# Performance work log

Measured on AMD Instinct MI355X. Metric: run time of the kernel, lower is better.

## Reference

```python
import jax, jax.numpy as jnp
import numpy as np

N_QUBITS = 16   # downsampled_size**2
N_KERNELS = 2
BSZ = 16        # hardcoded BATCH_SIZE in the repo
INV_SQRT2 = 0.70710678118654752


def ry_mat(theta):
    # RY(t) = [[cos(t/2), -sin(t/2)], [sin(t/2), cos(t/2)]]; theta: scalar or any batch shape
    c = jnp.cos(theta / 2)
    s = jnp.sin(theta / 2)
    m = jnp.stack([jnp.stack([c, -s], -1), jnp.stack([s, c], -1)], -2)
    return m.astype(jnp.complex64)


def rx_mat(theta):
    # RX(t) = [[cos(t/2), -i sin(t/2)], [-i sin(t/2), cos(t/2)]]
    c = jnp.cos(theta / 2).astype(jnp.complex64)
    s = jnp.sin(theta / 2).astype(jnp.complex64)
    return jnp.stack([jnp.stack([c, -1j * s], -1), jnp.stack([-1j * s, c], -1)], -2)


def apply_1q(state, U, w, n):
    # state: (b, 2**n) complex; U: (2,2) or (b,2,2); wire 0 = most significant bit
    b = state.shape[0]
    dl, dr = 1 << w, 1 << (n - 1 - w)
    s = state.reshape(b, dl, 2, dr)
    if U.ndim == 2:
        s = jnp.einsum('ab,xLbR->xLaR', U, s)
    else:
        s = jnp.einsum('xab,xLbR->xLaR', U, s)
    return s.reshape(b, -1)


def apply_cnot(state, c, t, n):
    # flip target axis where control bit == 1
    b = state.shape[0]
    st = state.reshape((b,) + (2,) * n)
    flipped = jnp.flip(st, axis=1 + t)
    mshape = [1] * (n + 1)
    mshape[1 + c] = 2
    ctrl = jnp.arange(2).reshape(mshape)
    st = jnp.where(ctrl == 1, flipped, st)
    return st.reshape(b, -1)


def quantum_model(xd, kernel_params):
    # xd: (b, 16) angles; kernel_params: (n_kernels, 5)
    b = xd.shape[0]
    n = N_QUBITS
    N = 1 << n
    bits = (jnp.arange(N)[:, None] >> jnp.arange(n - 1, -1, -1)[None, :]) & 1
    signs = (1 - 2 * bits).astype(jnp.float32)  # (N, n), PauliZ eigenvalues per wire
    enc = ry_mat(xd)  # (b, 16, 2, 2)
    outs = []
    for k in range(N_KERNELS):
        p = kernel_params[k]
        state = jnp.zeros((b, N), jnp.complex64).at[:, 0].set(1.0)
        # encoder: RY(x_i) on wire i
        for w in range(n):
            state = apply_1q(state, enc[:, w], w, n)
        # QuantumConvolution block (shared 5 trainable angles)
        ry0, ry1, ry2 = ry_mat(p[0]), ry_mat(p[1]), ry_mat(p[2])
        rx0, rx1 = rx_mat(p[3]), rx_mat(p[4])
        for i in range(n - 4):
            state = apply_1q(state, ry0, i, n)
            state = apply_cnot(state, i, i + 3, n)
            state = apply_1q(state, ry1, i + 3, n)
            state = apply_1q(state, ry2, i + 1, n)
            state = apply_cnot(state, i + 1, i + 4, n)
            state = apply_cnot(state, i + 3, i + 1, n)
            state = apply_1q(state, rx0, i + 4, n)
            state = apply_1q(state, rx1, i + 1, n)
        for i in range(n - 4):
            state = apply_cnot(state, i + 1, i, n)
            state = apply_cnot(state, i + 3, i, n)
            state = apply_cnot(state, i + 4, i, n)
        probs = state.real ** 2 + state.imag ** 2  # (b, N)
        expz = probs @ signs                        # (b, n)
        outs.append(expz[:, :-4])                   # drop last 4 wires
    return jnp.concatenate(outs, axis=1)            # (b, n_kernels*(n-4)) = (b, 24)


def setup_inputs() -> dict:
    key = jax.random.key(0)
    ks = jax.random.split(key, 8)
    return {
        'x': jax.random.normal(ks[0], (BSZ, 1, 28, 28), jnp.float32),
        'kernel_params': jax.random.uniform(ks[1], (N_KERNELS, 5), jnp.float32) * (2 * np.pi),
        'fc1_w': jax.random.normal(ks[2], (128, 24), jnp.float32) * 0.1,
        'fc1_b': jnp.zeros((128,), jnp.float32),
        'fc2_w': jax.random.normal(ks[3], (64, 128), jnp.float32) * 0.1,
        'fc2_b': jnp.zeros((64,), jnp.float32),
        'fc3_w': jax.random.normal(ks[4], (4, 64), jnp.float32) * 0.1,
        'fc3_b': jnp.zeros((4,), jnp.float32),
    }


def reference(x, kernel_params, fc1_w, fc1_b, fc2_w, fc2_b, fc3_w, fc3_b):
    b = x.shape[0]
    # AvgPool2d(kernel=7, stride=7): 28x28 -> 4x4, then flatten -> 16 features
    xd = x.reshape(b, 1, 4, 7, 4, 7).mean(axis=(3, 5)).reshape(b, 16)
    feats = quantum_model(xd, kernel_params)       # (b, 24)
    h = jax.nn.relu(feats @ fc1_w.T + fc1_b)
    h = jax.nn.relu(h @ fc2_w.T + fc2_b)
    return h @ fc3_w.T + fc3_b                      # (b, 4)
```

## Files before the change

kernel.cpp:

```cpp
#include <hip/hip_runtime.h>
#include <math.h>

typedef float2 cplx;
__device__ __forceinline__ cplx mk(float r, float i){ return make_float2(r, i); }

template<int B> struct LSH {
  static constexpr int v = (B==7)?0 : (B==8)?1 : (B==2)?2 : (B==1)?3 : (B==0)?4 : 5;
};

template<int PB>
__device__ __forceinline__ float lx(float v){
  if constexpr (PB == 7)
    return __int_as_float(__builtin_amdgcn_update_dpp(
        __float_as_int(v), __float_as_int(v), 0xB1, 0xF, 0xF, false));
  else if constexpr (PB == 8)
    return __int_as_float(__builtin_amdgcn_update_dpp(
        __float_as_int(v), __float_as_int(v), 0x4E, 0xF, 0xF, false));
  else if constexpr (PB == 2)
    return __int_as_float(__builtin_amdgcn_ds_swizzle(__float_as_int(v), 0x101F));
  else if constexpr (PB == 1)
    return __int_as_float(__builtin_amdgcn_ds_swizzle(__float_as_int(v), 0x201F));
  else if constexpr (PB == 0)
    return __int_as_float(__builtin_amdgcn_ds_swizzle(__float_as_int(v), 0x401F));
  else
    return __shfl_xor(v, 32, 64);
}

template<int PB, int CB, bool ISRX>
__device__ __forceinline__ void gate_pass(cplx* A, float c, float s, int lane)
{
  if constexpr (PB >= 3 && PB <= 6) {
    constexpr int RM = 1 << (PB - 3);
    bool cl = false;
    if constexpr (CB >= 0 && !(CB >= 3 && CB <= 6))
      cl = (lane >> LSH<CB>::v) & 1;
    #pragma unroll
    for (int r = 0; r < 16; ++r) {
      if (r & RM) continue;
      cplx a0 = A[r], a1 = A[r | RM];
      bool sw;
      if constexpr (CB < 0) sw = false;
      else if constexpr (CB >= 3 && CB <= 6) sw = (r >> (CB - 3)) & 1;
      else sw = cl;
      float i0x = sw ? a1.x : a0.x, i0y = sw ? a1.y : a0.y;
      float i1x = sw ? a0.x : a1.x, i1y = sw ? a0.y : a1.y;
      if constexpr (ISRX) {
        A[r]      = mk(fmaf(s, i1y, c*i0x), fmaf(-s, i1x, c*i0y));
        A[r | RM] = mk(fmaf(s, i0y, c*i1x), fmaf(-s, i0x, c*i1y));
      } else {
        A[r]      = mk(fmaf(-s, i1x, c*i0x), fmaf(-s, i1y, c*i0y));
        A[r | RM] = mk(fmaf( s, i0x, c*i1x), fmaf( s, i0y, c*i1y));
      }
    }
  } else {
    const int mybit = (lane >> LSH<PB>::v) & 1;
    const float ssy = mybit ? s : -s;
    #pragma unroll
    for (int r = 0; r < 16; ++r) {
      float px = lx<PB>(A[r].x);
      float py = lx<PB>(A[r].y);
      bool sw = false;
      if constexpr (CB >= 3 && CB <= 6) sw = (r >> (CB - 3)) & 1;
      float ox = A[r].x, oy = A[r].y;
      float ux = sw ? px : ox, uy = sw ? py : oy;
      float vx = sw ? ox : px, vy = sw ? oy : py;
      if constexpr (ISRX) A[r] = mk(fmaf(s, vy, c*ux), fmaf(-s, vx, c*uy));
      else                A[r] = mk(fmaf(ssy, vx, c*ux), fmaf(ssy, vy, c*uy));
    }
  }
}

template<int LO>
__device__ __forceinline__ void iter_reg(cplx* A, int lane,
    float c0,float s0,float c1,float s1,float c2,float s2,
    float cx,float sx,float c4,float s4)
{
  gate_pass<LO+4, -1,   false>(A, c0, s0, lane);
  gate_pass<LO+1, LO+4, false>(A, c1, s1, lane);
  gate_pass<LO+3, -1,   false>(A, c2, s2, lane);
  gate_pass<LO,   LO+3, true >(A, cx, sx, lane);
  gate_pass<LO+3, LO+1, true >(A, c4, s4, lane);
}

#define RUN6(A) \
  iter_reg<5>(A, lane, hc0,hs0,hc1,hs1,hc2,hs2,hcx,hsx,hc4,hs4); \
  iter_reg<4>(A, lane, hc0,hs0,hc1,hs1,hc2,hs2,hcx,hsx,hc4,hs4); \
  iter_reg<3>(A, lane, hc0,hs0,hc1,hs1,hc2,hs2,hcx,hsx,hc4,hs4); \
  iter_reg<2>(A, lane, hc0,hs0,hc1,hs1,hc2,hs2,hcx,hsx,hc4,hs4); \
  iter_reg<1>(A, lane, hc0,hs0,hc1,hs1,hc2,hs2,hcx,hsx,hc4,hs4); \
  iter_reg<0>(A, lane, hc0,hs0,hc1,hs1,hc2,hs2,hcx,hsx,hc4,hs4);

__device__ __forceinline__ float wave_sum(float v){
  v += lx<7>(v);
  v += lx<8>(v);
  v += lx<2>(v);
  v += lx<1>(v);
  v += lx<0>(v);
  v += __shfl_xor(v, 32, 64);
  return v;
}

__global__ __launch_bounds__(256) void sim_kernel(
    const float* __restrict__ x, const float* __restrict__ kp,
    float* __restrict__ pacc)
{
  __shared__ __align__(16) float lds[8320];

  const int tid = threadIdx.x, wv = tid >> 6, lane = tid & 63;
  const int gw = blockIdx.x * 4 + wv;
  const int pair = gw >> 6;
  const int chunk = gw & 63;
  const int b = pair & 15, k = pair >> 4;

  cplx*  P    = (cplx*)&lds[wv * 2048];
  float* angw = &lds[8192 + wv * 32];

  {
    int a = lane >> 2, q = lane & 3;
    int ii = a >> 2, jj = a & 3;
    const float* xb = x + b*784 + ii*7*28 + jj*7;
    float s = 0.f;
    for (int e = q; e < 49; e += 4) s += xb[(e/7)*28 + (e%7)];
    s += __shfl_xor(s, 1, 64);
    s += __shfl_xor(s, 2, 64);
    float ang = s * (1.0f/49.0f) * 0.5f;
    if (q == 0){ angw[a*2] = cosf(ang); angw[a*2+1] = sinf(ang); }
  }

  const float* p5 = kp + k*5;
  float hc0 = cosf(p5[0]*0.5f), hs0 = sinf(p5[0]*0.5f);
  float hc1 = cosf(p5[1]*0.5f), hs1 = sinf(p5[1]*0.5f);
  float hc2 = cosf(p5[2]*0.5f), hs2 = sinf(p5[2]*0.5f);
  float hcx = cosf(p5[3]*0.5f), hsx = sinf(p5[3]*0.5f);
  float hc4 = cosf(p5[4]*0.5f), hs4 = sinf(p5[4]*0.5f);

  __threadfence_block();

  cplx A[16];

  {
    float lp = 1.f;
    lp *= ((lane>>5)&1) ? angw[1]  : angw[0];
    lp *= ((lane>>1)&1) ? angw[3]  : angw[2];
    lp *= ( lane    &1) ? angw[5]  : angw[4];
    lp *= ((lane>>2)&1) ? angw[15] : angw[14];
    lp *= ((lane>>3)&1) ? angw[17] : angw[16];
    lp *= ((lane>>4)&1) ? angw[19] : angw[18];
    float c3 = angw[6],  s3 = angw[7];
    float c4w= angw[8],  s4w= angw[9];
    float c5 = angw[10], s5 = angw[11];
    float c6 = angw[12], s6 = angw[13];
    #pragma unroll
    for (int r = 0; r < 16; ++r){
      float rp = ((r&8)? s3:c3) * ((r&4)? s4w:c4w) * ((r&2)? s5:c5) * ((r&1)? s6:c6);
      A[r] = mk(lp * rp, 0.f);
    }
  }
  RUN6(A);

  #pragma unroll
  for (int r = 0; r < 16; ++r) P[(r << 6) | lane] = A[r];
  __threadfence_block();
  {
    int jc = (((lane>>5)&1) << 2) | (((lane>>1)&1) << 1) | (lane & 1);
    int h0 = (chunk << 4) | (jc << 1);
    int r0_ = (h0 >> 3) & 15;
    int l0_ = ((h0>>7)&1) | (((h0>>8)&1)<<1) | (((h0>>2)&1)<<2)
            | (((h0>>1)&1)<<3) | ((h0&1)<<4) | (((h0>>9)&1)<<5);
    cplx ps0 = P[(r0_ << 6) | l0_];
    cplx ps1 = P[(r0_ << 6) | l0_ | 16];

    float c10 = angw[20], s10 = angw[21];
    float c11 = angw[22], s11 = angw[23];
    float c12 = angw[24], s12 = angw[25];
    float preL = 1.f;
    preL *= ((lane>>2)&1) ? angw[27] : angw[26];
    preL *= ((lane>>3)&1) ? angw[29] : angw[28];
    preL *= ((lane>>4)&1) ? angw[31] : angw[30];
    #pragma unroll
    for (int r = 0; r < 16; ++r){
      float f = preL * (((r&4)? s10:c10) * ((r&2)? s11:c11) * ((r&1)? s12:c12));
      cplx v = (r & 8) ? ps1 : ps0;
      A[r] = mk(v.x * f, v.y * f);
    }
  }

  RUN6(A);

  {
    int idx_hi = (chunk << 10)
      | (((lane>>5)&1) << 9) | (((lane>>1)&1) << 8) | ((lane & 1) << 7)
      | (((lane>>2)&1) << 2) | (((lane>>3)&1) << 1) | ((lane>>4)&1);
    float p[16];
    #pragma unroll
    for (int r = 0; r < 16; ++r) p[r] = A[r].x*A[r].x + A[r].y*A[r].y;
    float out12[12];
    #pragma unroll
    for (int w = 0; w < 12; ++w){
      float s = 0.f;
      #pragma unroll
      for (int r = 0; r < 16; ++r)
        s += (__popc((r << 3) & (27 << (11 - w))) & 1) ? -p[r] : p[r];
      s = (__popc(idx_hi & (27 << (11 - w))) & 1) ? -s : s;
      out12[w] = wave_sum(s);
    }
    if (lane == 0){
      float4* dst = (float4*)(pacc + gw*12);
      dst[0] = make_float4(out12[0], out12[1], out12[2],  out12[3]);
      dst[1] = make_float4(out12[4], out12[5], out12[6],  out12[7]);
      dst[2] = make_float4(out12[8], out12[9], out12[10], out12[11]);
    }
  }
}

__global__ __launch_bounds__(256) void mlp_kernel(
    const float* __restrict__ pacc,
    const float* __restrict__ w1, const float* __restrict__ b1,
    const float* __restrict__ w2, const float* __restrict__ b2,
    const float* __restrict__ w3, const float* __restrict__ b3,
    float* __restrict__ out)
{
  __shared__ float feats[16*24];
  __shared__ float h1[16*128];
  __shared__ float h2[16*64];
  int tid = threadIdx.x;

  {
    int pr = tid >> 3, part = tid & 7;
    float sm[12];
    #pragma unroll
    for (int w = 0; w < 12; ++w) sm[w] = 0.f;
    for (int c = part; c < 64; c += 8){
      const float4* row = (const float4*)(pacc + (pr*64 + c)*12);
      float4 r0 = row[0], r1 = row[1], r2 = row[2];
      sm[0]+=r0.x; sm[1]+=r0.y; sm[2] +=r0.z; sm[3] +=r0.w;
      sm[4]+=r1.x; sm[5]+=r1.y; sm[6] +=r1.z; sm[7] +=r1.w;
      sm[8]+=r2.x; sm[9]+=r2.y; sm[10]+=r2.z; sm[11]+=r2.w;
    }
    #pragma unroll
    for (int m = 1; m < 8; m <<= 1)
      #pragma unroll
      for (int w = 0; w < 12; ++w)
        sm[w] += __shfl_xor(sm[w], m, 64);
    if (part == 0){
      int bb = pr & 15, kk = pr >> 4;
      #pragma unroll
      for (int w = 0; w < 12; ++w)
        feats[bb*24 + kk*12 + w] = sm[w];
    }
  }
  __syncthreads();

  for (int e = tid; e < 2048; e += 256){
    int bb = e >> 7, j = e & 127;
    const float4* wr = (const float4*)(w1 + j*24);
    const float4* fr = (const float4*)(feats + bb*24);
    float s = b1[j];
    #pragma unroll
    for (int q = 0; q < 6; ++q){
      float4 a = fr[q], w4 = wr[q];
      s += a.x*w4.x + a.y*w4.y + a.z*w4.z + a.w*w4.w;
    }
    h1[e] = fmaxf(s, 0.f);
  }
  __syncthreads();
  for (int e = tid; e < 1024; e += 256){
    int bb = e >> 6, j = e & 63;
    const float4* wr = (const float4*)(w2 + j*128);
    const float4* hr = (const float4*)(h1 + bb*128);
    float s = b2[j];
    #pragma unroll
    for (int q = 0; q < 32; ++q){
      float4 a = hr[q], w4 = wr[q];
      s += a.x*w4.x + a.y*w4.y + a.z*w4.z + a.w*w4.w;
    }
    h2[e] = fmaxf(s, 0.f);
  }
  __syncthreads();
  if (tid < 64){
    int bb = tid >> 2, j = tid & 3;
    const float4* wr = (const float4*)(w3 + j*64);
    const float4* hr = (const float4*)(h2 + bb*64);
    float s = b3[j];
    #pragma unroll
    for (int q = 0; q < 16; ++q){
      float4 a = hr[q], w4 = wr[q];
      s += a.x*w4.x + a.y*w4.y + a.z*w4.z + a.w*w4.w;
    }
    out[tid] = s;
  }
}

extern "C" void kernel_launch(void* const* d_in, const int* in_sizes, int n_in,
                              void* d_out, int out_size, void* d_ws, size_t ws_size,
                              hipStream_t stream) {
  const float* x  = (const float*)d_in[0];
  const float* kp = (const float*)d_in[1];
  const float* w1 = (const float*)d_in[2];
  const float* b1 = (const float*)d_in[3];
  const float* w2 = (const float*)d_in[4];
  const float* b2 = (const float*)d_in[5];
  const float* w3 = (const float*)d_in[6];
  const float* b3 = (const float*)d_in[7];
  float* out  = (float*)d_out;
  float* pacc = (float*)d_ws;

  sim_kernel<<<512, 256, 0, stream>>>(x, kp, pacc);
  mlp_kernel<<<1, 256, 0, stream>>>(pacc, w1, b1, w2, b2, w3, b3, out);
}
```

Before: 101.3 us.

## Pack gate math into v_pk_fma, reduce partials per block, parallelize MLP per batch

Replaces the scalar complex gate arithmetic with packed f32 inline asm (v_pk_mul/v_pk_fma) to halve VALU instruction count in the state-vector gate passes. The sim kernel now sums its four waves' partial expectations in LDS before writing one row per block, and the MLP kernel runs one block per batch element instead of a single block. The input pooling loop is also unrolled by rows. Hand-written op_sel/neg modifiers risk sign or lane errors, and the added __syncthreads is a new barrier.

```diff
diff --git a/kernel.cpp b/kernel.cpp
--- a/kernel.cpp
+++ b/kernel.cpp
@@ -1,8 +1,38 @@
 #include <hip/hip_runtime.h>
 #include <math.h>
 
-typedef float2 cplx;
-__device__ __forceinline__ cplx mk(float r, float i){ return make_float2(r, i); }
+typedef __attribute__((ext_vector_type(2))) float f2;
+
+__device__ __forceinline__ f2 pk_mul_c(f2 cs, f2 a){
+  f2 d;
+  asm("v_pk_mul_f32 %0, %1, %2 op_sel:[0,0] op_sel_hi:[0,1]"
+      : "=v"(d) : "v"(cs), "v"(a));
+  return d;
+}
+__device__ __forceinline__ f2 pk_fma_s(f2 cs, f2 b, f2 t){
+  f2 d;
+  asm("v_pk_fma_f32 %0, %1, %2, %3 op_sel:[1,0,0] op_sel_hi:[1,1,1]"
+      : "=v"(d) : "v"(cs), "v"(b), "v"(t));
+  return d;
+}
+__device__ __forceinline__ f2 pk_fma_ns(f2 cs, f2 b, f2 t){
+  f2 d;
+  asm("v_pk_fma_f32 %0, %1, %2, %3 op_sel:[1,0,0] op_sel_hi:[1,1,1] neg_lo:[1,0,0] neg_hi:[1,0,0]"
+      : "=v"(d) : "v"(cs), "v"(b), "v"(t));
+  return d;
+}
+__device__ __forceinline__ f2 pk_fma_sxn(f2 cs, f2 b, f2 t){
+  f2 d;
+  asm("v_pk_fma_f32 %0, %1, %2, %3 op_sel:[1,1,0] op_sel_hi:[1,0,1] neg_hi:[0,1,0]"
+      : "=v"(d) : "v"(cs), "v"(b), "v"(t));
+  return d;
+}
+__device__ __forceinline__ f2 pk_fma_lo(f2 w, f2 b, f2 t){
+  f2 d;
+  asm("v_pk_fma_f32 %0, %1, %2, %3 op_sel:[0,0,0] op_sel_hi:[0,1,1]"
+      : "=v"(d) : "v"(w), "v"(b), "v"(t));
+  return d;
+}
 
 template<int B> struct LSH {
   static constexpr int v = (B==7)?0 : (B==8)?1 : (B==2)?2 : (B==1)?3 : (B==0)?4 : 5;
@@ -27,7 +57,7 @@
 }
 
 template<int PB, int CB, bool ISRX>
-__device__ __forceinline__ void gate_pass(cplx* A, float c, float s, int lane)
+__device__ __forceinline__ void gate_pass(f2* A, f2 cs, int lane)
 {
   if constexpr (PB >= 3 && PB <= 6) {
     constexpr int RM = 1 << (PB - 3);
@@ -37,58 +67,63 @@
     #pragma unroll
     for (int r = 0; r < 16; ++r) {
       if (r & RM) continue;
-      cplx a0 = A[r], a1 = A[r | RM];
+      f2 a0 = A[r], a1 = A[r | RM];
       bool sw;
       if constexpr (CB < 0) sw = false;
       else if constexpr (CB >= 3 && CB <= 6) sw = (r >> (CB - 3)) & 1;
       else sw = cl;
-      float i0x = sw ? a1.x : a0.x, i0y = sw ? a1.y : a0.y;
-      float i1x = sw ? a0.x : a1.x, i1y = sw ? a0.y : a1.y;
+      f2 i0, i1;
+      i0.x = sw ? a1.x : a0.x;  i0.y = sw ? a1.y : a0.y;
+      i1.x = sw ? a0.x : a1.x;  i1.y = sw ? a0.y : a1.y;
       if constexpr (ISRX) {
-        A[r]      = mk(fmaf(s, i1y, c*i0x), fmaf(-s, i1x, c*i0y));
-        A[r | RM] = mk(fmaf(s, i0y, c*i1x), fmaf(-s, i0x, c*i1y));
+        A[r]      = pk_fma_sxn(cs, i1, pk_mul_c(cs, i0));
+        A[r | RM] = pk_fma_sxn(cs, i0, pk_mul_c(cs, i1));
       } else {
-        A[r]      = mk(fmaf(-s, i1x, c*i0x), fmaf(-s, i1y, c*i0y));
-        A[r | RM] = mk(fmaf( s, i0x, c*i1x), fmaf( s, i0y, c*i1y));
+        A[r]      = pk_fma_ns(cs, i1, pk_mul_c(cs, i0));
+        A[r | RM] = pk_fma_s (cs, i0, pk_mul_c(cs, i1));
       }
     }
   } else {
     const int mybit = (lane >> LSH<PB>::v) & 1;
-    const float ssy = mybit ? s : -s;
+    f2 sv;
+    if constexpr (!ISRX) {
+      float ssy = mybit ? cs.y : -cs.y;
+      sv.x = ssy; sv.y = ssy;
+    }
     #pragma unroll
     for (int r = 0; r < 16; ++r) {
-      float px = lx<PB>(A[r].x);
-      float py = lx<PB>(A[r].y);
+      f2 p;
+      p.x = lx<PB>(A[r].x);
+      p.y = lx<PB>(A[r].y);
       bool sw = false;
       if constexpr (CB >= 3 && CB <= 6) sw = (r >> (CB - 3)) & 1;
-      float ox = A[r].x, oy = A[r].y;
-      float ux = sw ? px : ox, uy = sw ? py : oy;
-      float vx = sw ? ox : px, vy = sw ? oy : py;
-      if constexpr (ISRX) A[r] = mk(fmaf(s, vy, c*ux), fmaf(-s, vx, c*uy));
-      else                A[r] = mk(fmaf(ssy, vx, c*ux), fmaf(ssy, vy, c*uy));
+      f2 u, v;
+      u.x = sw ? p.x : A[r].x;  u.y = sw ? p.y : A[r].y;
+      v.x = sw ? A[r].x : p.x;  v.y = sw ? A[r].y : p.y;
+      if constexpr (ISRX) A[r] = pk_fma_sxn(cs, v, pk_mul_c(cs, u));
+      else                A[r] = pk_fma_lo (sv, v, pk_mul_c(cs, u));
     }
   }
 }
 
 template<int LO>
-__device__ __forceinline__ void iter_reg(cplx* A, int lane,
-    float c0,float s0,float c1,float s1,float c2,float s2,
-    float cx,float sx,float c4,float s4)
+__device__ __forceinline__ void iter_reg(f2* A, int lane,
+    f2 cs0, f2 cs1, f2 cs2, f2 csx, f2 cs4)
 {
-  gate_pass<LO+4, -1,   false>(A, c0, s0, lane);
-  gate_pass<LO+1, LO+4, false>(A, c1, s1, lane);
-  gate_pass<LO+3, -1,   false>(A, c2, s2, lane);
-  gate_pass<LO,   LO+3, true >(A, cx, sx, lane);
-  gate_pass<LO+3, LO+1, true >(A, c4, s4, lane);
+  gate_pass<LO+4, -1,   false>(A, cs0, lane);
+  gate_pass<LO+1, LO+4, false>(A, cs1, lane);
+  gate_pass<LO+3, -1,   false>(A, cs2, lane);
+  gate_pass<LO,   LO+3, true >(A, csx, lane);
+  gate_pass<LO+3, LO+1, true >(A, cs4, lane);
 }
 
 #define RUN6(A) \
-  iter_reg<5>(A, lane, hc0,hs0,hc1,hs1,hc2,hs2,hcx,hsx,hc4,hs4); \
-  iter_reg<4>(A, lane, hc0,hs0,hc1,hs1,hc2,hs2,hcx,hsx,hc4,hs4); \
-  iter_reg<3>(A, lane, hc0,hs0,hc1,hs1,hc2,hs2,hcx,hsx,hc4,hs4); \
-  iter_reg<2>(A, lane, hc0,hs0,hc1,hs1,hc2,hs2,hcx,hsx,hc4,hs4); \
-  iter_reg<1>(A, lane, hc0,hs0,hc1,hs1,hc2,hs2,hcx,hsx,hc4,hs4); \
-  iter_reg<0>(A, lane, hc0,hs0,hc1,hs1,hc2,hs2,hcx,hsx,hc4,hs4);
+  iter_reg<5>(A, lane, cs0,cs1,cs2,csx,cs4); \
+  iter_reg<4>(A, lane, cs0,cs1,cs2,csx,cs4); \
+  iter_reg<3>(A, lane, cs0,cs1,cs2,csx,cs4); \
+  iter_reg<2>(A, lane, cs0,cs1,cs2,csx,cs4); \
+  iter_reg<1>(A, lane, cs0,cs1,cs2,csx,cs4); \
+  iter_reg<0>(A, lane, cs0,cs1,cs2,csx,cs4);
 
 __device__ __forceinline__ float wave_sum(float v){
   v += lx<7>(v);
@@ -104,7 +139,7 @@
     const float* __restrict__ x, const float* __restrict__ kp,
     float* __restrict__ pacc)
 {
-  __shared__ __align__(16) float lds[8320];
+  __shared__ __align__(16) float lds[8368];
 
   const int tid = threadIdx.x, wv = tid >> 6, lane = tid & 63;
   const int gw = blockIdx.x * 4 + wv;
@@ -112,15 +147,20 @@
   const int chunk = gw & 63;
   const int b = pair & 15, k = pair >> 4;
 
-  cplx*  P    = (cplx*)&lds[wv * 2048];
+  f2*    P    = (f2*)&lds[wv * 2048];
   float* angw = &lds[8192 + wv * 32];
+  float* stg  = &lds[8320];
 
   {
     int a = lane >> 2, q = lane & 3;
     int ii = a >> 2, jj = a & 3;
     const float* xb = x + b*784 + ii*7*28 + jj*7;
-    float s = 0.f;
-    for (int e = q; e < 49; e += 4) s += xb[(e/7)*28 + (e%7)];
+    const float* r0 = xb + q*28;
+    float s = r0[0]+r0[1]+r0[2]+r0[3]+r0[4]+r0[5]+r0[6];
+    if (q < 3){
+      const float* r1 = xb + (q+4)*28;
+      s += r1[0]+r1[1]+r1[2]+r1[3]+r1[4]+r1[5]+r1[6];
+    }
     s += __shfl_xor(s, 1, 64);
     s += __shfl_xor(s, 2, 64);
     float ang = s * (1.0f/49.0f) * 0.5f;
@@ -128,15 +168,16 @@
   }
 
   const float* p5 = kp + k*5;
-  float hc0 = cosf(p5[0]*0.5f), hs0 = sinf(p5[0]*0.5f);
-  float hc1 = cosf(p5[1]*0.5f), hs1 = sinf(p5[1]*0.5f);
-  float hc2 = cosf(p5[2]*0.5f), hs2 = sinf(p5[2]*0.5f);
-  float hcx = cosf(p5[3]*0.5f), hsx = sinf(p5[3]*0.5f);
-  float hc4 = cosf(p5[4]*0.5f), hs4 = sinf(p5[4]*0.5f);
+  f2 cs0, cs1, cs2, csx, cs4;
+  cs0.x = cosf(p5[0]*0.5f); cs0.y = sinf(p5[0]*0.5f);
+  cs1.x = cosf(p5[1]*0.5f); cs1.y = sinf(p5[1]*0.5f);
+  cs2.x = cosf(p5[2]*0.5f); cs2.y = sinf(p5[2]*0.5f);
+  csx.x = cosf(p5[3]*0.5f); csx.y = sinf(p5[3]*0.5f);
+  cs4.x = cosf(p5[4]*0.5f); cs4.y = sinf(p5[4]*0.5f);
 
   __threadfence_block();
 
-  cplx A[16];
+  f2 A[16];
 
   {
     float lp = 1.f;
@@ -153,7 +194,7 @@
     #pragma unroll
     for (int r = 0; r < 16; ++r){
       float rp = ((r&8)? s3:c3) * ((r&4)? s4w:c4w) * ((r&2)? s5:c5) * ((r&1)? s6:c6);
-      A[r] = mk(lp * rp, 0.f);
+      A[r].x = lp * rp; A[r].y = 0.f;
     }
   }
   RUN6(A);
@@ -167,8 +208,8 @@
     int r0_ = (h0 >> 3) & 15;
     int l0_ = ((h0>>7)&1) | (((h0>>8)&1)<<1) | (((h0>>2)&1)<<2)
             | (((h0>>1)&1)<<3) | ((h0&1)<<4) | (((h0>>9)&1)<<5);
-    cplx ps0 = P[(r0_ << 6) | l0_];
-    cplx ps1 = P[(r0_ << 6) | l0_ | 16];
+    f2 ps0 = P[(r0_ << 6) | l0_];
+    f2 ps1 = P[(r0_ << 6) | l0_ | 16];
 
     float c10 = angw[20], s10 = angw[21];
     float c11 = angw[22], s11 = angw[23];
@@ -180,13 +221,14 @@
     #pragma unroll
     for (int r = 0; r < 16; ++r){
       float f = preL * (((r&4)? s10:c10) * ((r&2)? s11:c11) * ((r&1)? s12:c12));
-      cplx v = (r & 8) ? ps1 : ps0;
-      A[r] = mk(v.x * f, v.y * f);
+      f2 v = (r & 8) ? ps1 : ps0;
+      A[r].x = v.x * f; A[r].y = v.y * f;
     }
   }
 
   RUN6(A);
 
+  float out12[12];
   {
     int idx_hi = (chunk << 10)
       | (((lane>>5)&1) << 9) | (((lane>>1)&1) << 8) | ((lane & 1) << 7)
@@ -194,7 +236,6 @@
     float p[16];
     #pragma unroll
     for (int r = 0; r < 16; ++r) p[r] = A[r].x*A[r].x + A[r].y*A[r].y;
-    float out12[12];
     #pragma unroll
     for (int w = 0; w < 12; ++w){
       float s = 0.f;
@@ -204,12 +245,16 @@
       s = (__popc(idx_hi & (27 << (11 - w))) & 1) ? -s : s;
       out12[w] = wave_sum(s);
     }
-    if (lane == 0){
-      float4* dst = (float4*)(pacc + gw*12);
-      dst[0] = make_float4(out12[0], out12[1], out12[2],  out12[3]);
-      dst[1] = make_float4(out12[4], out12[5], out12[6],  out12[7]);
-      dst[2] = make_float4(out12[8], out12[9], out12[10], out12[11]);
-    }
+  }
+
+  if (lane == 0){
+    #pragma unroll
+    for (int w = 0; w < 12; ++w) stg[wv*12 + w] = out12[w];
+  }
+  __syncthreads();
+  if (wv == 0 && lane < 12){
+    float t = stg[lane] + stg[12+lane] + stg[24+lane] + stg[36+lane];
+    pacc[blockIdx.x*12 + lane] = t;
   }
 }
 
@@ -220,74 +265,60 @@
     const float* __restrict__ w3, const float* __restrict__ b3,
     float* __restrict__ out)
 {
-  __shared__ float feats[16*24];
-  __shared__ float h1[16*128];
-  __shared__ float h2[16*64];
-  int tid = threadIdx.x;
-
-  {
-    int pr = tid >> 3, part = tid & 7;
-    float sm[12];
-    #pragma unroll
-    for (int w = 0; w < 12; ++w) sm[w] = 0.f;
-    for (int c = part; c < 64; c += 8){
-      const float4* row = (const float4*)(pacc + (pr*64 + c)*12);
-      float4 r0 = row[0], r1 = row[1], r2 = row[2];
-      sm[0]+=r0.x; sm[1]+=r0.y; sm[2] +=r0.z; sm[3] +=r0.w;
-      sm[4]+=r1.x; sm[5]+=r1.y; sm[6] +=r1.z; sm[7] +=r1.w;
-      sm[8]+=r2.x; sm[9]+=r2.y; sm[10]+=r2.z; sm[11]+=r2.w;
-    }
-    #pragma unroll
-    for (int m = 1; m < 8; m <<= 1)
-      #pragma unroll
-      for (int w = 0; w < 12; ++w)
-        sm[w] += __shfl_xor(sm[w], m, 64);
-    if (part == 0){
-      int bb = pr & 15, kk = pr >> 4;
-      #pragma unroll
-      for (int w = 0; w < 12; ++w)
-        feats[bb*24 + kk*12 + w] = sm[w];
+  __shared__ __align__(16) float feats[24];
+  __shared__ __align__(16) float h1[128];
+  __shared__ __align__(16) float h2[64];
+  const int tid = threadIdx.x, b = blockIdx.x;
+
+  {
+    int f = tid >> 3, part = tid & 7;
+    if (f < 24){
+      int kk = (f >= 12) ? 1 : 0, w = f - kk*12;
+      int pair = kk*16 + b;
+      const float* base = pacc + pair*16*12 + w;
+      float s = base[part*12] + base[(part+8)*12];
+      s += __shfl_xor(s, 1, 64);
+      s += __shfl_xor(s, 2, 64);
+      s += __shfl_xor(s, 4, 64);
+      if (part == 0) feats[f] = s;
     }
   }
   __syncthreads();
 
-  for (int e = tid; e < 2048; e += 256){
-    int bb = e >> 7, j = e & 127;
-    const float4* wr = (const float4*)(w1 + j*24);
-    const float4* fr = (const float4*)(feats + bb*24);
-    float s = b1[j];
+  if (tid < 128){
+    const float4* wr = (const float4*)(w1 + tid*24);
+    const float4* fr = (const float4*)feats;
+    float s = b1[tid];
     #pragma unroll
     for (int q = 0; q < 6; ++q){
-      float4 a = fr[q], w4 = wr[q];
-      s += a.x*w4.x + a.y*w4.y + a.z*w4.z + a.w*w4.w;
-    }
-    h1[e] = fmaxf(s, 0.f);
-  }
-  __syncthreads();
-  for (int e = tid; e < 1024; e += 256){
-    int bb = e >> 6, j = e & 63;
-    const float4* wr = (const float4*)(w2 + j*128);
-    const float4* hr = (const float4*)(h1 + bb*128);
-    float s = b2[j];
-    #pragma unroll
-    for (int q = 0; q < 32; ++q){
-      float4 a = hr[q], w4 = wr[q];
-      s += a.x*w4.x + a.y*w4.y + a.z*w4.z + a.w*w4.w;
-    }
-    h2[e] = fmaxf(s, 0.f);
+      float4 a = fr[q], ww = wr[q];
+      s += a.x*ww.x + a.y*ww.y + a.z*ww.z + a.w*ww.w;
+    }
+    h1[tid] = fmaxf(s, 0.f);
   }
   __syncthreads();
   if (tid < 64){
-    int bb = tid >> 2, j = tid & 3;
-    const float4* wr = (const float4*)(w3 + j*64);
-    const float4* hr = (const float4*)(h2 + bb*64);
-    float s = b3[j];
+    const float4* wr = (const float4*)(w2 + tid*128);
+    const float4* hr = (const float4*)h1;
+    float s = b2[tid];
+    #pragma unroll
+    for (int q = 0; q < 32; ++q){
+      float4 a = hr[q], ww = wr[q];
+      s += a.x*ww.x + a.y*ww.y + a.z*ww.z + a.w*ww.w;
+    }
+    h2[tid] = fmaxf(s, 0.f);
+  }
+  __syncthreads();
+  if (tid < 4){
+    const float4* wr = (const float4*)(w3 + tid*64);
+    const float4* hr = (const float4*)h2;
+    float s = b3[tid];
     #pragma unroll
     for (int q = 0; q < 16; ++q){
-      float4 a = hr[q], w4 = wr[q];
-      s += a.x*w4.x + a.y*w4.y + a.z*w4.z + a.w*w4.w;
-    }
-    out[tid] = s;
+      float4 a = hr[q], ww = wr[q];
+      s += a.x*ww.x + a.y*ww.y + a.z*ww.z + a.w*ww.w;
+    }
+    out[b*4 + tid] = s;
   }
 }
 
@@ -306,5 +337,5 @@
   float* pacc = (float*)d_ws;
 
   sim_kernel<<<512, 256, 0, stream>>>(x, kp, pacc);
-  mlp_kernel<<<1, 256, 0, stream>>>(pacc, w1, b1, w2, b2, w3, b3, out);
-}
+  mlp_kernel<<<16, 256, 0, stream>>>(pacc, w1, b1, w2, b2, w3, b3, out);
+}
```

After: 89.55 us. 1.13x faster.
